# Kernel optimization log

Hardware: AMD Instinct MI355X
Metric: run time of the kernel (lower is better)

Reference implementation:

```python
import jax, jax.numpy as jnp
import numpy as np

IN_FEATURES = 1024
OUT_FEATURES = 1024
GRID_SIZE = 8
SPLINE_ORDER = 3
NUM_CTRL = GRID_SIZE + SPLINE_ORDER  # 11


def _make_grid():
    h = 2.0 / GRID_SIZE
    return jnp.linspace(-1.0 - SPLINE_ORDER * h, 1.0 + SPLINE_ORDER * h,
                        GRID_SIZE + 2 * SPLINE_ORDER + 1, dtype=jnp.float32)  # [15]


def b_splines(t, grid, order):
    # t: [B, F] (already tanh'd). Vectorized over all features at once —
    # the torch per-feature Python loop computes identical math per column.
    te = t[..., None]  # [B, F, 1]
    basis = ((te >= grid[:-1]) & (te < grid[1:])).astype(t.dtype)  # [B, F, G-1]
    for k in range(1, order + 1):
        left_den = grid[k:-1] - grid[:-k - 1]
        left_den = jnp.where(left_den == 0, jnp.ones_like(left_den), left_den)
        left = (te - grid[:-k - 1]) / left_den * basis[..., :-1]
        right_den = grid[k + 1:] - grid[1:-k]
        right_den = jnp.where(right_den == 0, jnp.ones_like(right_den), right_den)
        right = (grid[k + 1:] - te) / right_den * basis[..., 1:]
        basis = left + right
    return basis  # [B, F, NUM_CTRL]


def setup_inputs() -> dict:
    key = jax.random.key(0)
    kx, kc, kw = jax.random.split(key, 3)
    x = jax.random.normal(kx, (4096, IN_FEATURES), dtype=jnp.float32)
    coeffs = jax.random.normal(kc, (IN_FEATURES, OUT_FEATURES, NUM_CTRL), dtype=jnp.float32) * 0.05
    base_weight = jax.random.normal(kw, (IN_FEATURES, OUT_FEATURES), dtype=jnp.float32) * 0.05
    grid = _make_grid()
    return {"x": x, "coeffs": coeffs, "base_weight": base_weight, "grid": grid}


def reference(x, coeffs, base_weight, grid):
    bases = b_splines(jnp.tanh(x), grid, SPLINE_ORDER)          # [B, in, n]
    activation = jnp.einsum('bin,ion->bo', bases, coeffs)        # [B, out]
    residual = x @ base_weight                                   # [B, out]
    return activation + residual
```

## Files before the change

### kernel.cpp

```cpp
#include <hip/hip_runtime.h>
#include <hip/hip_bf16.h>

typedef __attribute__((ext_vector_type(8))) short bf16x8;
typedef __attribute__((ext_vector_type(4))) float f32x4;
typedef __attribute__((ext_vector_type(4))) unsigned short u16x4;
typedef __attribute__((ext_vector_type(8))) unsigned short u16x8;

#define M_DIM 4096
#define N_DIM 1024
#define IN_F  1024
#define K_DIM 12288
#define KSLICE 4
#define KPART (K_DIM / KSLICE)

__device__ __forceinline__ unsigned short f2b(float v) {
  __hip_bfloat16 h = __float2bfloat16(v);
  return *reinterpret_cast<unsigned short*>(&h);
}

__device__ __forceinline__ void spline12(float xv, float* w) {
  float t  = tanhf(xv);
  float tf = (t + 1.75f) * 4.0f;
  int j = (int)tf;
  j = j < 3 ? 3 : (j > 10 ? 10 : j);
  float u  = tf - (float)j;
  float um = 1.0f - u;
  float u2 = u * u;
  float w0 = um * um * um * (1.0f / 6.0f);
  float w1 = (0.5f * u - 1.0f) * u2 + (2.0f / 3.0f);
  float w2 = ((-0.5f * u + 0.5f) * u + 0.5f) * u + (1.0f / 6.0f);
  float w3 = u * u2 * (1.0f / 6.0f);
  int base = j - 3;
  #pragma unroll
  for (int s = 0; s < 11; ++s) {
    int r = s - base;
    w[s] = (r == 0) ? w0 : (r == 1) ? w1 : (r == 2) ? w2 : (r == 3) ? w3 : 0.0f;
  }
  w[11] = xv;
}

__global__ __launch_bounds__(256) void bases_kernel(const float* __restrict__ x,
                                                    unsigned short* __restrict__ A) {
  int idx = blockIdx.x * 256 + threadIdx.x;
  float xv = x[idx];
  float w[12];
  spline12(xv, w);
  unsigned short h[12];
  #pragma unroll
  for (int s = 0; s < 12; ++s) h[s] = f2b(w[s]);
  u16x4* dst = (u16x4*)(A + (size_t)idx * 12);
  dst[0] = (u16x4){h[0], h[1], h[2],  h[3]};
  dst[1] = (u16x4){h[4], h[5], h[6],  h[7]};
  dst[2] = (u16x4){h[8], h[9], h[10], h[11]};
}

__global__ __launch_bounds__(256) void repack_kernel(const float* __restrict__ coeffs,
                                                     const float* __restrict__ W,
                                                     unsigned short* __restrict__ Bt) {
  __shared__ float lc[64 * 176];
  __shared__ float lw[64 * 16];
  const int o0 = blockIdx.x * 16;
  const int i0 = blockIdx.y * 64;
  const int tid = threadIdx.x;
  #pragma unroll
  for (int it = 0; it < 11; ++it) {
    int v = it * 256 + tid;
    int i = v / 44, c = v - i * 44;
    f32x4 d = *(const f32x4*)(coeffs + ((size_t)(i0 + i) * 1024 + o0) * 11 + c * 4);
    *(f32x4*)(lc + i * 176 + c * 4) = d;
  }
  #pragma unroll
  for (int it = 0; it < 4; ++it) {
    int e = it * 256 + tid;
    int i = e >> 4, ol = e & 15;
    lw[e] = W[(size_t)(i0 + i) * 1024 + o0 + ol];
  }
  __syncthreads();
  #pragma unroll
  for (int it = 0; it < 6; ++it) {
    int v = it * 256 + tid;
    int ol = v / 96, c = v - ol * 96;
    unsigned short h[8];
    #pragma unroll
    for (int s = 0; s < 8; ++s) {
      int g = c * 8 + s;
      int i = g / 12, n = g - i * 12;
      float val = (n < 11) ? lc[i * 176 + ol * 11 + n] : lw[i * 16 + ol];
      h[s] = f2b(val);
    }
    *(u16x8*)(Bt + (size_t)(o0 + ol) * K_DIM + (size_t)i0 * 12 + c * 8) =
        (u16x8){h[0], h[1], h[2], h[3], h[4], h[5], h[6], h[7]};
  }
}

__device__ __forceinline__ void async16(const void* g, void* l) {
  __builtin_amdgcn_global_load_lds(
      (const __attribute__((address_space(1))) void*)g,
      (__attribute__((address_space(3))) void*)l, 16, 0, 0);
}

__global__ __launch_bounds__(256, 4) void gemm_kernel(const unsigned short* __restrict__ A,
                                                      const unsigned short* __restrict__ Bt,
                                                      float* __restrict__ out) {
  __shared__ __align__(16) unsigned short As[128 * 64];
  __shared__ __align__(16) unsigned short Bs[128 * 64];
  const int tid  = threadIdx.x;
  const int lane = tid & 63;
  const int wid  = tid >> 6;
  const int wm   = wid >> 1, wn = wid & 1;

  const int blk = blockIdx.x;
  const int xcd = blk & 7;
  const int idx = blk >> 3;
  const int ks  = idx & 3;
  const int q   = idx >> 2;
  const int bn  = q & 7;
  const int bm  = xcd * 4 + (q >> 3);
  const size_t m0 = (size_t)bm * 128;
  const size_t n0 = (size_t)bn * 128;
  const size_t kbyte = (size_t)ks * KPART * 2;

  const char* gA[4]; const char* gB[4];
  unsigned short* lA[4]; unsigned short* lB[4];
  #pragma unroll
  for (int p = 0; p < 4; ++p) {
    int rr  = (wid * 4 + p) * 8 + (lane >> 3);
    int c16 = (lane & 7) ^ (rr & 7);
    gA[p] = (const char*)A  + ((m0 + rr) * K_DIM) * 2 + kbyte + c16 * 16;
    gB[p] = (const char*)Bt + ((n0 + rr) * K_DIM) * 2 + kbyte + c16 * 16;
    lA[p] = As + (wid * 4 + p) * 512;
    lB[p] = Bs + (wid * 4 + p) * 512;
  }

  int offA[2][4], offB[2][4];
  #pragma unroll
  for (int kk = 0; kk < 2; ++kk) {
    #pragma unroll
    for (int m = 0; m < 4; ++m) {
      int row = wm * 64 + m * 16 + (lane & 15);
      int ck  = (kk * 4 + (lane >> 4)) ^ (row & 7);
      offA[kk][m] = row * 128 + ck * 16;
      int rowb = wn * 64 + m * 16 + (lane & 15);
      int ckb  = (kk * 4 + (lane >> 4)) ^ (rowb & 7);
      offB[kk][m] = rowb * 128 + ckb * 16;
    }
  }

  f32x4 acc[4][4];
  #pragma unroll
  for (int m = 0; m < 4; ++m)
    #pragma unroll
    for (int n = 0; n < 4; ++n) acc[m][n] = (f32x4){0.f, 0.f, 0.f, 0.f};

  for (int kt = 0; kt < KPART / 64; ++kt) {
    const size_t koff = (size_t)kt * 128;
    #pragma unroll
    for (int p = 0; p < 4; ++p) {
      async16(gA[p] + koff, lA[p]);
      async16(gB[p] + koff, lB[p]);
    }
    __syncthreads();
    #pragma unroll
    for (int kk = 0; kk < 2; ++kk) {
      bf16x8 a[4], b[4];
      #pragma unroll
      for (int m = 0; m < 4; ++m)
        a[m] = *(const bf16x8*)((const char*)As + offA[kk][m]);
      #pragma unroll
      for (int n = 0; n < 4; ++n)
        b[n] = *(const bf16x8*)((const char*)Bs + offB[kk][n]);
      #pragma unroll
      for (int m = 0; m < 4; ++m)
        #pragma unroll
        for (int n = 0; n < 4; ++n)
          acc[m][n] = __builtin_amdgcn_mfma_f32_16x16x32_bf16(a[m], b[n], acc[m][n], 0, 0, 0);
    }
    __syncthreads();
  }

  const int lr = (lane >> 4) * 4;
  const int lc = lane & 15;
  #pragma unroll
  for (int m = 0; m < 4; ++m)
    #pragma unroll
    for (int n = 0; n < 4; ++n)
      #pragma unroll
      for (int j = 0; j < 4; ++j)
        atomicAdd(&out[(m0 + wm * 64 + m * 16 + lr + j) * N_DIM + n0 + wn * 64 + n * 16 + lc],
                  acc[m][n][j]);
}

__global__ __launch_bounds__(256) void fallback_kernel(const float* __restrict__ x,
                                                       const float* __restrict__ coeffs,
                                                       const float* __restrict__ W,
                                                       float* __restrict__ out) {
  __shared__ float bas[16][64][12];
  const int o0 = blockIdx.x * 64;
  const int b0 = blockIdx.y * 16;
  const int tid = threadIdx.x;
  const int o = tid & 63, bg = tid >> 6;
  float acc[4] = {0.f, 0.f, 0.f, 0.f};
  for (int ic = 0; ic < 16; ++ic) {
    __syncthreads();
    #pragma unroll
    for (int p = 0; p < 4; ++p) {
      int pp = tid + p * 256;
      int bb = pp >> 6, il = pp & 63;
      float w[12];
      spline12(x[(size_t)(b0 + bb) * 1024 + ic * 64 + il], w);
      #pragma unroll
      for (int n = 0; n < 12; ++n) bas[bb][il][n] = w[n];
    }
    __syncthreads();
    for (int il = 0; il < 64; ++il) {
      int gi = ic * 64 + il;
      const float* cp = coeffs + ((size_t)gi * 1024 + o0 + o) * 11;
      float cf[12];
      #pragma unroll
      for (int n = 0; n < 11; ++n) cf[n] = cp[n];
      cf[11] = W[(size_t)gi * 1024 + o0 + o];
      #pragma unroll
      for (int bb = 0; bb < 4; ++bb) {
        float s = 0.f;
        #pragma unroll
        for (int n = 0; n < 12; ++n) s += bas[bg * 4 + bb][il][n] * cf[n];
        acc[bb] += s;
      }
    }
  }
  #pragma unroll
  for (int bb = 0; bb < 4; ++bb)
    out[(size_t)(b0 + bg * 4 + bb) * 1024 + o0 + o] = acc[bb];
}

extern "C" void kernel_launch(void* const* d_in, const int* in_sizes, int n_in,
                              void* d_out, int out_size, void* d_ws, size_t ws_size,
                              hipStream_t stream) {
  const float* x      = (const float*)d_in[0];
  const float* coeffs = (const float*)d_in[1];
  const float* W      = (const float*)d_in[2];
  float* out = (float*)d_out;

  const size_t needA = (size_t)M_DIM * K_DIM * 2;
  const size_t needB = (size_t)N_DIM * K_DIM * 2;

  if (ws_size >= needA + needB) {
    unsigned short* Abuf = (unsigned short*)d_ws;
    unsigned short* Btuf = (unsigned short*)((char*)d_ws + needA);
    hipMemsetAsync(out, 0, (size_t)out_size * sizeof(float), stream);
    bases_kernel<<<dim3(M_DIM * IN_F / 256), dim3(256), 0, stream>>>(x, Abuf);
    repack_kernel<<<dim3(64, 16), dim3(256), 0, stream>>>(coeffs, W, Btuf);
    gemm_kernel<<<dim3(32 * 8 * KSLICE), dim3(256), 0, stream>>>(Abuf, Btuf, out);
  } else {
    fallback_kernel<<<dim3(16, 256), dim3(256), 0, stream>>>(x, coeffs, W, out);
  }
}
```

Baseline: 272.9 us.

## Triple-buffer GEMM with async LDS prefetch, larger 256x128 tiles, two K-slices

Rewrites the GEMM main loop to keep three LDS stages in flight, using explicit vmcnt waits and raw barriers so global-to-LDS loads overlap MFMA work. The block tile grows to 256x128 with 512 threads (8 waves), and the K split drops from 4 to 2, which halves the atomic output traffic. The bases kernel now handles two elements per thread with wider stores. The trade-off is one block per CU because of the 144KB of LDS, plus fewer blocks overall (256), which may hurt latency hiding and load balance.

```diff
diff --git a/kernel.cpp b/kernel.cpp
--- a/kernel.cpp
+++ b/kernel.cpp
@@ -10,8 +10,10 @@
 #define N_DIM 1024
 #define IN_F  1024
 #define K_DIM 12288
-#define KSLICE 4
-#define KPART (K_DIM / KSLICE)
+#define KS2   2
+#define KPART2 (K_DIM / KS2)
+#define BK 64
+#define NT (KPART2 / BK)
 
 __device__ __forceinline__ unsigned short f2b(float v) {
   __hip_bfloat16 h = __float2bfloat16(v);
@@ -41,17 +43,18 @@
 
 __global__ __launch_bounds__(256) void bases_kernel(const float* __restrict__ x,
                                                     unsigned short* __restrict__ A) {
-  int idx = blockIdx.x * 256 + threadIdx.x;
-  float xv = x[idx];
-  float w[12];
-  spline12(xv, w);
-  unsigned short h[12];
-  #pragma unroll
-  for (int s = 0; s < 12; ++s) h[s] = f2b(w[s]);
-  u16x4* dst = (u16x4*)(A + (size_t)idx * 12);
-  dst[0] = (u16x4){h[0], h[1], h[2],  h[3]};
-  dst[1] = (u16x4){h[4], h[5], h[6],  h[7]};
-  dst[2] = (u16x4){h[8], h[9], h[10], h[11]};
+  int e0 = blockIdx.x * 512 + threadIdx.x * 2;
+  float2 xv = *(const float2*)(x + e0);
+  float w0[12], w1[12];
+  spline12(xv.x, w0);
+  spline12(xv.y, w1);
+  unsigned short h[24];
+  #pragma unroll
+  for (int s = 0; s < 12; ++s) { h[s] = f2b(w0[s]); h[12 + s] = f2b(w1[s]); }
+  u16x8* dst = (u16x8*)(A + (size_t)e0 * 12);
+  dst[0] = (u16x8){h[0],  h[1],  h[2],  h[3],  h[4],  h[5],  h[6],  h[7]};
+  dst[1] = (u16x8){h[8],  h[9],  h[10], h[11], h[12], h[13], h[14], h[15]};
+  dst[2] = (u16x8){h[16], h[17], h[18], h[19], h[20], h[21], h[22], h[23]};
 }
 
 __global__ __launch_bounds__(256) void repack_kernel(const float* __restrict__ coeffs,
@@ -99,38 +102,55 @@
       (__attribute__((address_space(3))) void*)l, 16, 0, 0);
 }
 
-__global__ __launch_bounds__(256, 4) void gemm_kernel(const unsigned short* __restrict__ A,
+__global__ __launch_bounds__(512, 1) void gemm_kernel(const unsigned short* __restrict__ A,
                                                       const unsigned short* __restrict__ Bt,
                                                       float* __restrict__ out) {
-  __shared__ __align__(16) unsigned short As[128 * 64];
-  __shared__ __align__(16) unsigned short Bs[128 * 64];
+  __shared__ __align__(16) unsigned short lds[73728];
+  char* lp = (char*)lds;
+  const int AS0 = 0, AS1 = 32768, AS2 = 65536;
+  const int BS0 = 98304, BS1 = 98304 + 16384, BS2 = 98304 + 32768;
+
   const int tid  = threadIdx.x;
   const int lane = tid & 63;
   const int wid  = tid >> 6;
-  const int wm   = wid >> 1, wn = wid & 1;
+  const int wm   = wid >> 1;
+  const int wn   = wid & 1;
 
   const int blk = blockIdx.x;
-  const int xcd = blk & 7;
-  const int idx = blk >> 3;
-  const int ks  = idx & 3;
-  const int q   = idx >> 2;
-  const int bn  = q & 7;
-  const int bm  = xcd * 4 + (q >> 3);
-  const size_t m0 = (size_t)bm * 128;
+  const int bn  = blk & 7;
+  const int r   = blk >> 3;
+  const int bm  = r & 15;
+  const int ks  = r >> 4;
+  const size_t m0 = (size_t)bm * 256;
   const size_t n0 = (size_t)bn * 128;
-  const size_t kbyte = (size_t)ks * KPART * 2;
-
-  const char* gA[4]; const char* gB[4];
-  unsigned short* lA[4]; unsigned short* lB[4];
-  #pragma unroll
-  for (int p = 0; p < 4; ++p) {
-    int rr  = (wid * 4 + p) * 8 + (lane >> 3);
-    int c16 = (lane & 7) ^ (rr & 7);
-    gA[p] = (const char*)A  + ((m0 + rr) * K_DIM) * 2 + kbyte + c16 * 16;
-    gB[p] = (const char*)Bt + ((n0 + rr) * K_DIM) * 2 + kbyte + c16 * 16;
-    lA[p] = As + (wid * 4 + p) * 512;
-    lB[p] = Bs + (wid * 4 + p) * 512;
-  }
+  const size_t ksbyte = (size_t)ks * KPART2 * 2;
+
+  const char* srcA[4]; int ldsA[4];
+  #pragma unroll
+  for (int q = 0; q < 4; ++q) {
+    int g = q * 512 + tid;
+    int rr = g >> 3, cp = g & 7;
+    int cs = cp ^ (rr & 7);
+    srcA[q] = (const char*)A + ((m0 + rr) * (size_t)K_DIM) * 2 + ksbyte + cs * 16;
+    ldsA[q] = g * 16;
+  }
+  const char* srcB[2]; int ldsB[2];
+  #pragma unroll
+  for (int q = 0; q < 2; ++q) {
+    int g = q * 512 + tid;
+    int rr = g >> 3, cp = g & 7;
+    int cs = cp ^ (rr & 7);
+    srcB[q] = (const char*)Bt + ((n0 + rr) * (size_t)K_DIM) * 2 + ksbyte + cs * 16;
+    ldsB[q] = g * 16;
+  }
+
+  auto stage = [&](int sa, int sb, int tile) {
+    size_t kb = (size_t)tile * 128;
+    #pragma unroll
+    for (int q = 0; q < 4; ++q) async16(srcA[q] + kb, lp + sa + ldsA[q]);
+    #pragma unroll
+    for (int q = 0; q < 2; ++q) async16(srcB[q] + kb, lp + sb + ldsB[q]);
+  };
 
   int offA[2][4], offB[2][4];
   #pragma unroll
@@ -140,9 +160,12 @@
       int row = wm * 64 + m * 16 + (lane & 15);
       int ck  = (kk * 4 + (lane >> 4)) ^ (row & 7);
       offA[kk][m] = row * 128 + ck * 16;
-      int rowb = wn * 64 + m * 16 + (lane & 15);
+    }
+    #pragma unroll
+    for (int n = 0; n < 4; ++n) {
+      int rowb = wn * 64 + n * 16 + (lane & 15);
       int ckb  = (kk * 4 + (lane >> 4)) ^ (rowb & 7);
-      offB[kk][m] = rowb * 128 + ckb * 16;
+      offB[kk][n] = rowb * 128 + ckb * 16;
     }
   }
 
@@ -152,30 +175,45 @@
     #pragma unroll
     for (int n = 0; n < 4; ++n) acc[m][n] = (f32x4){0.f, 0.f, 0.f, 0.f};
 
-  for (int kt = 0; kt < KPART / 64; ++kt) {
-    const size_t koff = (size_t)kt * 128;
-    #pragma unroll
-    for (int p = 0; p < 4; ++p) {
-      async16(gA[p] + koff, lA[p]);
-      async16(gB[p] + koff, lB[p]);
-    }
-    __syncthreads();
+  stage(AS0, BS0, 0);
+  stage(AS1, BS1, 1);
+  stage(AS2, BS2, 2);
+
+  int cA = AS0, nA = AS1, fA = AS2;
+  int cB = BS0, nB = BS1, fB = BS2;
+
+  for (int t = 0; t < NT; ++t) {
+    if (t < NT - 2)       asm volatile("s_waitcnt vmcnt(12)" ::: "memory");
+    else if (t == NT - 2) asm volatile("s_waitcnt vmcnt(6)"  ::: "memory");
+    else                  asm volatile("s_waitcnt vmcnt(0)"  ::: "memory");
+    __builtin_amdgcn_s_barrier();
+    __builtin_amdgcn_sched_barrier(0);
+    asm volatile("" ::: "memory");
+
+    __builtin_amdgcn_s_setprio(1);
     #pragma unroll
     for (int kk = 0; kk < 2; ++kk) {
       bf16x8 a[4], b[4];
       #pragma unroll
-      for (int m = 0; m < 4; ++m)
-        a[m] = *(const bf16x8*)((const char*)As + offA[kk][m]);
-      #pragma unroll
-      for (int n = 0; n < 4; ++n)
-        b[n] = *(const bf16x8*)((const char*)Bs + offB[kk][n]);
+      for (int m = 0; m < 4; ++m) a[m] = *(const bf16x8*)(lp + cA + offA[kk][m]);
+      #pragma unroll
+      for (int n = 0; n < 4; ++n) b[n] = *(const bf16x8*)(lp + cB + offB[kk][n]);
       #pragma unroll
       for (int m = 0; m < 4; ++m)
         #pragma unroll
         for (int n = 0; n < 4; ++n)
           acc[m][n] = __builtin_amdgcn_mfma_f32_16x16x32_bf16(a[m], b[n], acc[m][n], 0, 0, 0);
     }
-    __syncthreads();
+    __builtin_amdgcn_s_setprio(0);
+
+    asm volatile("" ::: "memory");
+    __builtin_amdgcn_sched_barrier(0);
+    __builtin_amdgcn_s_barrier();
+
+    if (t + 3 < NT) stage(cA, cB, t + 3);
+
+    int ta = cA; cA = nA; nA = fA; fA = ta;
+    int tb = cB; cB = nB; nB = fB; fB = tb;
   }
 
   const int lr = (lane >> 4) * 4;
@@ -248,9 +286,9 @@
     unsigned short* Abuf = (unsigned short*)d_ws;
     unsigned short* Btuf = (unsigned short*)((char*)d_ws + needA);
     hipMemsetAsync(out, 0, (size_t)out_size * sizeof(float), stream);
-    bases_kernel<<<dim3(M_DIM * IN_F / 256), dim3(256), 0, stream>>>(x, Abuf);
+    bases_kernel<<<dim3(M_DIM * IN_F / 512), dim3(256), 0, stream>>>(x, Abuf);
     repack_kernel<<<dim3(64, 16), dim3(256), 0, stream>>>(coeffs, W, Btuf);
-    gemm_kernel<<<dim3(32 * 8 * KSLICE), dim3(256), 0, stream>>>(Abuf, Btuf, out);
+    gemm_kernel<<<dim3(16 * 8 * KS2), dim3(512), 0, stream>>>(Abuf, Btuf, out);
   } else {
     fallback_kernel<<<dim3(16, 256), dim3(256), 0, stream>>>(x, coeffs, W, out);
   }
```

After: 276.7 us. About the same (+1.4%).
